# Kernel optimization log

Measured on AMD Instinct MI355X. Metric: run time of the kernel, lower is better.

The kernel has to match this reference:

```python
import jax, jax.numpy as jnp
import numpy as np

B, S, D_MODEL, H = 4, 2048, 2048, 16
HD = D_MODEL // H  # 128
ROPE_BASE = 10000.0


def apply_rope(x):
    # x: [B, H, S, HD]; interleaved-pair rotary embedding along seq axis
    s, d = x.shape[2], x.shape[3]
    inv_freq = 1.0 / (ROPE_BASE ** (jnp.arange(0, d, 2, dtype=jnp.float32) / d))  # [d/2]
    ang = jnp.arange(s, dtype=jnp.float32)[:, None] * inv_freq[None, :]  # [S, d/2]
    cos, sin = jnp.cos(ang), jnp.sin(ang)
    x0, x1 = x[..., 0::2], x[..., 1::2]  # [B,H,S,d/2]
    o0 = x0 * cos - x1 * sin
    o1 = x0 * sin + x1 * cos
    return jnp.stack([o0, o1], axis=-1).reshape(x.shape)


def setup_inputs() -> dict:
    key = jax.random.key(0)
    ks = jax.random.split(key, 5)
    sc = 1.0 / np.sqrt(D_MODEL)
    return {
        "x": jax.random.normal(ks[0], (B, S, D_MODEL), dtype=jnp.float32),
        "Wq": jax.random.normal(ks[1], (D_MODEL, D_MODEL), dtype=jnp.float32) * sc,
        "Wk": jax.random.normal(ks[2], (D_MODEL, D_MODEL), dtype=jnp.float32) * sc,
        "Wv": jax.random.normal(ks[3], (D_MODEL, D_MODEL), dtype=jnp.float32) * sc,
        "Wo": jax.random.normal(ks[4], (D_MODEL, D_MODEL), dtype=jnp.float32) * sc,
        "bo": jnp.zeros((D_MODEL,), dtype=jnp.float32),
    }


def reference(x, Wq, Wk, Wv, Wo, bo):
    b, s, _ = x.shape
    # torch Linear: y = x @ W.T (no qkv bias)
    q = (x @ Wq.T).reshape(b, s, H, HD).transpose(0, 2, 1, 3)  # [B,H,S,HD]
    k = (x @ Wk.T).reshape(b, s, H, HD).transpose(0, 2, 1, 3)
    v = (x @ Wv.T).reshape(b, s, H, HD).transpose(0, 2, 1, 3)
    q = apply_rope(q)
    k = apply_rope(k)
    scores = jnp.einsum("bhqd,bhkd->bhqk", q, k)
    causal = jnp.tril(jnp.ones((s, s), dtype=bool))
    scores = jnp.where(causal, scores, -jnp.inf)
    attn = jax.nn.softmax(scores / jnp.sqrt(jnp.float32(HD)), axis=-1)
    # dropout p=0.0 -> identity
    ctx = jnp.einsum("bhqk,bhkd->bqhd", attn, v).reshape(b, s, H * HD)
    return ctx @ Wo.T + bo
```

## Files before the change

### kernel.cpp

```cpp
#include <hip/hip_runtime.h>
#include <hip/hip_bf16.h>
#include <math.h>

#define B_  4
#define S_  2048
#define DM  2048
#define H_  16
#define HD_ 128

typedef __bf16 bf16;
typedef __bf16 bf16x4 __attribute__((ext_vector_type(4)));
typedef __bf16 bf16x8 __attribute__((ext_vector_type(8)));
typedef float  f32x4  __attribute__((ext_vector_type(4)));

__device__ __forceinline__ void gload_lds16(const bf16* g, bf16* l) {
  __builtin_amdgcn_global_load_lds(
      (const __attribute__((address_space(1))) void*)g,
      (__attribute__((address_space(3))) void*)l, 16, 0, 0);
}

__global__ void cast_f32_bf16(const float* __restrict__ src, bf16* __restrict__ dst, int n4) {
  int stride = gridDim.x * blockDim.x;
  for (int i = blockIdx.x * blockDim.x + threadIdx.x; i < n4; i += stride) {
    float4 v = reinterpret_cast<const float4*>(src)[i];
    bf16x4 o = { (bf16)v.x, (bf16)v.y, (bf16)v.z, (bf16)v.w };
    reinterpret_cast<bf16x4*>(dst)[i] = o;
  }
}

__global__ void rope_table_k(float* __restrict__ tab) {
  int idx = blockIdx.x * blockDim.x + threadIdx.x;
  if (idx >= S_ * (HD_ / 2)) return;
  int pos = idx >> 6, i = idx & 63;
  float inv = powf(10000.0f, -(2.0f * i) / (float)HD_);
  float ang = (float)pos * inv;
  tab[2 * idx]     = cosf(ang);
  tab[2 * idx + 1] = sinf(ang);
}

template<int EPI>
__global__ __launch_bounds__(512, 2)
void gemm8p(const bf16* __restrict__ A, const bf16* __restrict__ Bt,
            bf16* __restrict__ Oq, bf16* __restrict__ Ok, bf16* __restrict__ Ovt,
            float* __restrict__ Cf, const float* __restrict__ bias,
            const float* __restrict__ tab, int N, int K) {
  __shared__ char lds[131072];
  const int tid = threadIdx.x;
  const int w = tid >> 6, l = tid & 63;
  const int lr = l & 15, lg = l >> 4;
  const int wm = w >> 2, wn = w & 3;
  const int row0 = blockIdx.y * 256, col0 = blockIdx.x * 256;
  const int NT = K >> 6;

  auto stageSlot = [&](int isB, int kh, int kt2) {
    const bf16* src = isB ? (Bt + (size_t)col0 * K) : (A + (size_t)row0 * K);
    char* dstbase = (char*)lds + (kt2 & 1) * 65536 + isB * 32768 + kh * 16384;
    const int kcol = kt2 * 64 + kh * 32;
#pragma unroll
    for (int u = 0; u < 2; ++u) {
      int D = w * 2048 + u * 1024 + l * 16;
      int r = D >> 6, cb = D & 63;
      int sc = cb ^ (((r >> 1) & 3) << 4);
      gload_lds16(src + (size_t)r * K + kcol + (sc >> 1),
                  (bf16*)(dstbase + w * 2048 + u * 1024));
    }
  };

  const int swzt = ((lr >> 1) & 3) << 4;
  int offA[2][4], offB[4];
#pragma unroll
  for (int qm = 0; qm < 2; ++qm)
#pragma unroll
    for (int mi = 0; mi < 4; ++mi) {
      int r = wm * 128 + qm * 64 + mi * 16 + lr;
      offA[qm][mi] = r * 64 + ((lg * 16) ^ swzt);
    }
#pragma unroll
  for (int ni = 0; ni < 4; ++ni) {
    int r = wn * 64 + ni * 16 + lr;
    offB[ni] = 32768 + r * 64 + ((lg * 16) ^ swzt);
  }

  f32x4 acc[8][4] = {};

  stageSlot(0, 0, 0); stageSlot(1, 0, 0);
  stageSlot(0, 1, 0); stageSlot(1, 1, 0);
  if (NT > 1) { stageSlot(0, 0, 1); stageSlot(1, 0, 1); }

#pragma unroll 1
  for (int kt = 0; kt < NT; ++kt) {
    const char* bufb = (const char*)lds + (kt & 1) * 65536;
#pragma unroll
    for (int q = 0; q < 4; ++q) {
      const int qm = q & 1 ? 1 : 0;
      const int kh = q >> 1;
      const int qmm = (q == 1 || q == 3) ? 1 : 0;
      if (q == 0) {
        if (kt + 1 < NT) asm volatile("s_waitcnt vmcnt(8)" ::: "memory");
        else             asm volatile("s_waitcnt vmcnt(4)" ::: "memory");
        __builtin_amdgcn_s_barrier();
      } else if (q == 2) {
        if (kt + 1 < NT) asm volatile("s_waitcnt vmcnt(8)" ::: "memory");
        else             asm volatile("s_waitcnt vmcnt(0)" ::: "memory");
        __builtin_amdgcn_s_barrier();
      }
      const char* bb = bufb + kh * 16384;
      bf16x8 af[4], bfr[4];
#pragma unroll
      for (int mi = 0; mi < 4; ++mi)
        af[mi] = *reinterpret_cast<const bf16x8*>(bb + offA[qmm][mi]);
#pragma unroll
      for (int ni = 0; ni < 4; ++ni)
        bfr[ni] = *reinterpret_cast<const bf16x8*>(bb + offB[ni]);
      if (q < 2) { if (kt + 1 < NT) stageSlot(q & 1, 1, kt + 1); }
      else       { if (kt + 2 < NT) stageSlot(q & 1, 0, kt + 2); }
      __builtin_amdgcn_s_barrier();
      asm volatile("s_waitcnt lgkmcnt(0)" ::: "memory");
      __builtin_amdgcn_s_setprio(1);
#pragma unroll
      for (int mi = 0; mi < 4; ++mi)
#pragma unroll
        for (int ni = 0; ni < 4; ++ni)
          acc[qmm * 4 + mi][ni] =
              __builtin_amdgcn_mfma_f32_16x16x32_bf16(af[mi], bfr[ni], acc[qmm * 4 + mi][ni], 0, 0, 0);
      __builtin_amdgcn_s_setprio(0);
    }
  }

#pragma unroll
  for (int ai = 0; ai < 8; ++ai) {
    int rb = row0 + wm * 128 + ai * 16 + lg * 4;
#pragma unroll
    for (int ni = 0; ni < 4; ++ni) {
      int gc = col0 + wn * 64 + ni * 16 + lr;
      if (EPI == 1) {
#pragma unroll
        for (int j = 0; j < 4; ++j)
          Cf[(size_t)(rb + j) * N + gc] = acc[ai][ni][j] + bias[gc];
      } else {
        int reg = col0 >> 11;
        int cc = gc & 2047;
        if (reg == 2) {
          int bb2 = rb >> 11, s = rb & 2047;
          int hh = cc >> 7, dd = cc & 127;
          bf16x4 pack = { (bf16)acc[ai][ni][0], (bf16)acc[ai][ni][1],
                          (bf16)acc[ai][ni][2], (bf16)acc[ai][ni][3] };
          *reinterpret_cast<bf16x4*>(Ovt + (((size_t)(bb2 * H_ + hh) * HD_ + dd) << 11) + s) = pack;
        } else {
          bf16* Dst = (reg == 0) ? Oq : Ok;
          float scale = (reg == 0) ? 0.08838834764831845f : 1.0f;
          int i2 = (cc & 127) >> 1;
          float sgn = (lr & 1) ? 1.0f : -1.0f;
#pragma unroll
          for (int j = 0; j < 4; ++j) {
            float own = acc[ai][ni][j];
            float par = __shfl_xor(own, 1);
            int s = (rb + j) & (S_ - 1);
            float2 cs = reinterpret_cast<const float2*>(tab)[s * 64 + i2];
            Dst[(size_t)(rb + j) * 2048 + cc] = (bf16)((own * cs.x + sgn * par * cs.y) * scale);
          }
        }
      }
    }
  }
}

__global__ __launch_bounds__(512, 4)
void attn_fwd(const bf16* __restrict__ Q, const bf16* __restrict__ K,
              const bf16* __restrict__ Vt, bf16* __restrict__ O) {
  __shared__ bf16 Ks[2][64 * 128];
  __shared__ bf16 Vs[2][128 * 64];
  __shared__ bf16 Ps[8][16 * 64];
  const int tid = threadIdx.x;
  const int w = tid >> 6, l = tid & 63;
  const int lr = l & 15, lg = l >> 4;
  const int bx = blockIdx.x;
  const int h = blockIdx.y, b = blockIdx.z;
  const size_t bbase = (size_t)b * S_ * DM + (size_t)h * HD_;
  const bf16* vtb = Vt + (size_t)(b * H_ + h) * HD_ * S_;

#pragma unroll 1
  for (int pass = 0; pass < 2; ++pass) {
    const int qt = pass ? bx : (15 - bx);
    const int q0 = qt * 128 + w * 16;
    const int ktmax = 2 * qt + 1;

    bf16x8 qf[4];
#pragma unroll
    for (int kb = 0; kb < 4; ++kb)
      qf[kb] = *reinterpret_cast<const bf16x8*>(Q + bbase + (size_t)(q0 + lr) * DM + kb * 32 + lg * 8);

    float m_r = -INFINITY;
    float l_r = 0.f;
    f32x4 o[8] = {};

#pragma unroll
    for (int i = 0; i < 2; ++i) {
      int X = w * 2048 + i * 1024 + l * 16;
      int r = X >> 8, scb = (X & 255) ^ ((r & 7) << 4);
      gload_lds16(K + bbase + (size_t)r * DM + (scb >> 1), &Ks[0][(w * 2048 + i * 1024) >> 1]);
    }
#pragma unroll
    for (int i = 0; i < 2; ++i) {
      int X = w * 2048 + i * 1024 + l * 16;
      int d = X >> 7, scb = (X & 127) ^ ((d & 7) << 4);
      gload_lds16(vtb + (size_t)d * S_ + (scb >> 1), &Vs[0][(w * 2048 + i * 1024) >> 1]);
    }

    for (int kt = 0; kt <= ktmax; ++kt) {
      const int buf = kt & 1;
      if (kt < ktmax) {
        const int nk = (kt + 1) * 64;
#pragma unroll
        for (int i = 0; i < 2; ++i) {
          int X = w * 2048 + i * 1024 + l * 16;
          int r = X >> 8, scb = (X & 255) ^ ((r & 7) << 4);
          gload_lds16(K + bbase + (size_t)(nk + r) * DM + (scb >> 1),
                      &Ks[buf ^ 1][(w * 2048 + i * 1024) >> 1]);
        }
#pragma unroll
        for (int i = 0; i < 2; ++i) {
          int X = w * 2048 + i * 1024 + l * 16;
          int d = X >> 7, scb = (X & 127) ^ ((d & 7) << 4);
          gload_lds16(vtb + (size_t)d * S_ + nk + (scb >> 1),
                      &Vs[buf ^ 1][(w * 2048 + i * 1024) >> 1]);
        }
        asm volatile("s_waitcnt vmcnt(4)" ::: "memory");
      } else {
        asm volatile("s_waitcnt vmcnt(0)" ::: "memory");
      }
      __builtin_amdgcn_s_barrier();

      f32x4 sc4[4];
      __builtin_amdgcn_s_setprio(1);
#pragma unroll
      for (int cb = 0; cb < 4; ++cb) {
        sc4[cb] = f32x4{0.f, 0.f, 0.f, 0.f};
        int r = cb * 16 + lr;
#pragma unroll
        for (int kb = 0; kb < 4; ++kb) {
          int off = r * 256 + ((kb * 64 + lg * 16) ^ ((lr & 7) << 4));
          bf16x8 kf = *reinterpret_cast<const bf16x8*>((const char*)Ks[buf] + off);
          sc4[cb] = __builtin_amdgcn_mfma_f32_16x16x32_bf16(kf, qf[kb], sc4[cb], 0, 0, 0);
        }
      }
      __builtin_amdgcn_s_setprio(0);

      const int kv0 = kt * 64;
      if (kv0 + 63 > q0) {
        const int qq = q0 + lr;
#pragma unroll
        for (int cb = 0; cb < 4; ++cb)
#pragma unroll
          for (int jj = 0; jj < 4; ++jj)
            if (kv0 + cb * 16 + lg * 4 + jj > qq) sc4[cb][jj] = -INFINITY;
      }

      float tm = -INFINITY;
#pragma unroll
      for (int cb = 0; cb < 4; ++cb)
#pragma unroll
        for (int jj = 0; jj < 4; ++jj) tm = fmaxf(tm, sc4[cb][jj]);
      tm = fmaxf(tm, __shfl_xor(tm, 16));
      tm = fmaxf(tm, __shfl_xor(tm, 32));
      float mnew = fmaxf(m_r, tm);
      float sc_f = __expf(m_r - mnew);
      m_r = mnew;
      float rs = 0.f;
#pragma unroll
      for (int cb = 0; cb < 4; ++cb)
#pragma unroll
        for (int jj = 0; jj < 4; ++jj) {
          float p = __expf(sc4[cb][jj] - mnew);
          sc4[cb][jj] = p;
          rs += p;
        }
      rs += __shfl_xor(rs, 16);
      rs += __shfl_xor(rs, 32);
      l_r = l_r * sc_f + rs;

      float scO[4];
#pragma unroll
      for (int j = 0; j < 4; ++j) scO[j] = __shfl(sc_f, lg * 4 + j);
#pragma unroll
      for (int nb = 0; nb < 8; ++nb)
#pragma unroll
        for (int j = 0; j < 4; ++j) o[nb][j] *= scO[j];

#pragma unroll
      for (int cb = 0; cb < 4; ++cb) {
        bf16x4 pk = { (bf16)sc4[cb][0], (bf16)sc4[cb][1], (bf16)sc4[cb][2], (bf16)sc4[cb][3] };
        int off = lr * 128 + ((cb * 32 + lg * 8) ^ ((lr & 7) << 4));
        *reinterpret_cast<bf16x4*>((char*)Ps[w] + off) = pk;
      }

      bf16x8 pf[2];
#pragma unroll
      for (int kc = 0; kc < 2; ++kc) {
        int off = lr * 128 + ((kc * 64 + lg * 16) ^ ((lr & 7) << 4));
        pf[kc] = *reinterpret_cast<const bf16x8*>((const char*)Ps[w] + off);
      }
      __builtin_amdgcn_s_setprio(1);
#pragma unroll
      for (int nb = 0; nb < 8; ++nb) {
        int d = nb * 16 + lr;
#pragma unroll
        for (int kc = 0; kc < 2; ++kc) {
          int off = d * 128 + ((kc * 64 + lg * 16) ^ ((lr & 7) << 4));
          bf16x8 vf = *reinterpret_cast<const bf16x8*>((const char*)Vs[buf] + off);
          o[nb] = __builtin_amdgcn_mfma_f32_16x16x32_bf16(pf[kc], vf, o[nb], 0, 0, 0);
        }
      }
      __builtin_amdgcn_s_setprio(0);

      asm volatile("s_waitcnt lgkmcnt(0)" ::: "memory");
      __builtin_amdgcn_s_barrier();
    }

    float lO[4];
#pragma unroll
    for (int j = 0; j < 4; ++j) lO[j] = __shfl(l_r, lg * 4 + j);
#pragma unroll
    for (int j = 0; j < 4; ++j) {
      float inv = 1.0f / lO[j];
      size_t rowoff = bbase + (size_t)(q0 + lg * 4 + j) * DM;
#pragma unroll
      for (int nb = 0; nb < 8; ++nb)
        O[rowoff + nb * 16 + lr] = (bf16)(o[nb][j] * inv);
    }
  }
}

extern "C" void kernel_launch(void* const* d_in, const int* in_sizes, int n_in,
                              void* d_out, int out_size, void* d_ws, size_t ws_size,
                              hipStream_t stream) {
  const float* x  = (const float*)d_in[0];
  const float* Wq = (const float*)d_in[1];
  const float* Wk = (const float*)d_in[2];
  const float* Wv = (const float*)d_in[3];
  const float* Wo = (const float*)d_in[4];
  const float* bo = (const float*)d_in[5];
  float* out = (float*)d_out;

  const size_t NX = (size_t)B_ * S_ * DM;
  const size_t NW = (size_t)DM * DM;
  char* ws = (char*)d_ws;
  bf16* xb   = (bf16*)ws; ws += NX * 2;
  bf16* wqkv = (bf16*)ws; ws += 3 * NW * 2;
  bf16* wob  = (bf16*)ws; ws += NW * 2;
  bf16* qb   = (bf16*)ws; ws += NX * 2;
  bf16* kb   = (bf16*)ws; ws += NX * 2;
  bf16* vt   = (bf16*)ws; ws += NX * 2;
  bf16* ctxb = (bf16*)ws; ws += NX * 2;
  float* tab = (float*)ws; ws += (size_t)S_ * 64 * 2 * sizeof(float);

  cast_f32_bf16<<<(int)((NX / 4 + 255) / 256), 256, 0, stream>>>(x, xb, (int)(NX / 4));
  cast_f32_bf16<<<(int)((NW / 4 + 255) / 256), 256, 0, stream>>>(Wq, wqkv, (int)(NW / 4));
  cast_f32_bf16<<<(int)((NW / 4 + 255) / 256), 256, 0, stream>>>(Wk, wqkv + NW, (int)(NW / 4));
  cast_f32_bf16<<<(int)((NW / 4 + 255) / 256), 256, 0, stream>>>(Wv, wqkv + 2 * NW, (int)(NW / 4));
  cast_f32_bf16<<<(int)((NW / 4 + 255) / 256), 256, 0, stream>>>(Wo, wob, (int)(NW / 4));
  rope_table_k<<<(S_ * 64 + 255) / 256, 256, 0, stream>>>(tab);

  const int M = B_ * S_;
  gemm8p<0><<<dim3(3 * DM / 256, M / 256), 512, 0, stream>>>(
      xb, wqkv, qb, kb, vt, nullptr, nullptr, tab, 3 * DM, DM);

  attn_fwd<<<dim3(8, H_, B_), 512, 0, stream>>>(qb, kb, vt, ctxb);

  gemm8p<1><<<dim3(DM / 256, M / 256), 512, 0, stream>>>(
      ctxb, wob, nullptr, nullptr, nullptr, out, bo, nullptr, DM, DM);
}
```

Before: 438.8 us.

## Fuse casts, add XCD-aware block remapping, and lazy softmax rescaling

Merges the five f32-to-bf16 cast launches into a single grid-stride kernel. Remaps GEMM and attention block indices so neighbouring tiles land on the same XCD for better L2 reuse. Skips the online-softmax max update and output rescale when the new tile max stays within a threshold of the running max. Also drops an explicit lgkmcnt wait before the MFMA loop. The wait removal relies on the compiler inserting the needed LDS waits, and the lazy rescale allows exp values up to e^8 before renormalisation, which slightly changes numerics.

Result: faster. 418.4 us (-4.6%).

```diff
diff --git a/kernel.cpp b/kernel.cpp
--- a/kernel.cpp
+++ b/kernel.cpp
@@ -19,12 +19,28 @@
       (__attribute__((address_space(3))) void*)l, 16, 0, 0);
 }
 
-__global__ void cast_f32_bf16(const float* __restrict__ src, bf16* __restrict__ dst, int n4) {
+#define NX4 4194304
+#define NW4 1048576
+__global__ void cast_all(const float* __restrict__ x, const float* __restrict__ wq,
+                         const float* __restrict__ wk, const float* __restrict__ wv,
+                         const float* __restrict__ wo,
+                         bf16* __restrict__ xb, bf16* __restrict__ wqkv,
+                         bf16* __restrict__ wob) {
+  const int total = NX4 + 4 * NW4;
   int stride = gridDim.x * blockDim.x;
-  for (int i = blockIdx.x * blockDim.x + threadIdx.x; i < n4; i += stride) {
-    float4 v = reinterpret_cast<const float4*>(src)[i];
+  for (int i = blockIdx.x * blockDim.x + threadIdx.x; i < total; i += stride) {
+    const float* src; bf16* dst; int j;
+    if (i < NX4) { src = x; dst = xb; j = i; }
+    else {
+      int t = i - NX4; int r = t >> 20; j = t & (NW4 - 1);
+      if      (r == 0) { src = wq; dst = wqkv; }
+      else if (r == 1) { src = wk; dst = wqkv + (size_t)NW4 * 4; }
+      else if (r == 2) { src = wv; dst = wqkv + (size_t)NW4 * 8; }
+      else             { src = wo; dst = wob; }
+    }
+    float4 v = reinterpret_cast<const float4*>(src)[j];
     bf16x4 o = { (bf16)v.x, (bf16)v.y, (bf16)v.z, (bf16)v.w };
-    reinterpret_cast<bf16x4*>(dst)[i] = o;
+    reinterpret_cast<bf16x4*>(dst)[j] = o;
   }
 }
 
@@ -49,7 +65,13 @@
   const int w = tid >> 6, l = tid & 63;
   const int lr = l & 15, lg = l >> 4;
   const int wm = w >> 2, wn = w & 3;
-  const int row0 = blockIdx.y * 256, col0 = blockIdx.x * 256;
+  const int L = blockIdx.x + gridDim.x * blockIdx.y;
+  const int xcd = L & 7, s = L >> 3;
+  const int rpx = gridDim.y >> 3;
+  const int qq_ = s / gridDim.x;
+  const int by = xcd * rpx + qq_;
+  const int bx = s - qq_ * gridDim.x;
+  const int row0 = by * 256, col0 = bx * 256;
   const int NT = K >> 6;
 
   auto stageSlot = [&](int isB, int kh, int kt2) {
@@ -92,9 +114,8 @@
     const char* bufb = (const char*)lds + (kt & 1) * 65536;
 #pragma unroll
     for (int q = 0; q < 4; ++q) {
-      const int qm = q & 1 ? 1 : 0;
       const int kh = q >> 1;
-      const int qmm = (q == 1 || q == 3) ? 1 : 0;
+      const int qmm = (q & 1);
       if (q == 0) {
         if (kt + 1 < NT) asm volatile("s_waitcnt vmcnt(8)" ::: "memory");
         else             asm volatile("s_waitcnt vmcnt(4)" ::: "memory");
@@ -115,7 +136,6 @@
       if (q < 2) { if (kt + 1 < NT) stageSlot(q & 1, 1, kt + 1); }
       else       { if (kt + 2 < NT) stageSlot(q & 1, 0, kt + 2); }
       __builtin_amdgcn_s_barrier();
-      asm volatile("s_waitcnt lgkmcnt(0)" ::: "memory");
       __builtin_amdgcn_s_setprio(1);
 #pragma unroll
       for (int mi = 0; mi < 4; ++mi)
@@ -141,11 +161,11 @@
         int reg = col0 >> 11;
         int cc = gc & 2047;
         if (reg == 2) {
-          int bb2 = rb >> 11, s = rb & 2047;
+          int bb2 = rb >> 11, ss = rb & 2047;
           int hh = cc >> 7, dd = cc & 127;
           bf16x4 pack = { (bf16)acc[ai][ni][0], (bf16)acc[ai][ni][1],
                           (bf16)acc[ai][ni][2], (bf16)acc[ai][ni][3] };
-          *reinterpret_cast<bf16x4*>(Ovt + (((size_t)(bb2 * H_ + hh) * HD_ + dd) << 11) + s) = pack;
+          *reinterpret_cast<bf16x4*>(Ovt + (((size_t)(bb2 * H_ + hh) * HD_ + dd) << 11) + ss) = pack;
         } else {
           bf16* Dst = (reg == 0) ? Oq : Ok;
           float scale = (reg == 0) ? 0.08838834764831845f : 1.0f;
@@ -155,8 +175,8 @@
           for (int j = 0; j < 4; ++j) {
             float own = acc[ai][ni][j];
             float par = __shfl_xor(own, 1);
-            int s = (rb + j) & (S_ - 1);
-            float2 cs = reinterpret_cast<const float2*>(tab)[s * 64 + i2];
+            int ss = (rb + j) & (S_ - 1);
+            float2 cs = reinterpret_cast<const float2*>(tab)[ss * 64 + i2];
             Dst[(size_t)(rb + j) * 2048 + cc] = (bf16)((own * cs.x + sgn * par * cs.y) * scale);
           }
         }
@@ -174,8 +194,11 @@
   const int tid = threadIdx.x;
   const int w = tid >> 6, l = tid & 63;
   const int lr = l & 15, lg = l >> 4;
-  const int bx = blockIdx.x;
-  const int h = blockIdx.y, b = blockIdx.z;
+  const int L = blockIdx.x + 8 * (blockIdx.y + 16 * blockIdx.z);
+  const int xcd = L & 7, s = L >> 3;
+  const int p = xcd * 8 + (s & 7);
+  const int bx = s >> 3;
+  const int h = p & 15, b = p >> 4;
   const size_t bbase = (size_t)b * S_ * DM + (size_t)h * HD_;
   const bf16* vtb = Vt + (size_t)(b * H_ + h) * HD_ * S_;
 
@@ -263,29 +286,34 @@
         for (int jj = 0; jj < 4; ++jj) tm = fmaxf(tm, sc4[cb][jj]);
       tm = fmaxf(tm, __shfl_xor(tm, 16));
       tm = fmaxf(tm, __shfl_xor(tm, 32));
-      float mnew = fmaxf(m_r, tm);
-      float sc_f = __expf(m_r - mnew);
-      m_r = mnew;
+      const bool resc = !__all(tm <= m_r + 8.0f);
+      float sc_f = 1.f;
+      if (resc) {
+        float mnew = fmaxf(m_r, tm);
+        sc_f = __expf(m_r - mnew);
+        m_r = mnew;
+      }
       float rs = 0.f;
 #pragma unroll
       for (int cb = 0; cb < 4; ++cb)
 #pragma unroll
         for (int jj = 0; jj < 4; ++jj) {
-          float p = __expf(sc4[cb][jj] - mnew);
-          sc4[cb][jj] = p;
-          rs += p;
+          float pp = __expf(sc4[cb][jj] - m_r);
+          sc4[cb][jj] = pp;
+          rs += pp;
         }
       rs += __shfl_xor(rs, 16);
       rs += __shfl_xor(rs, 32);
       l_r = l_r * sc_f + rs;
-
-      float scO[4];
-#pragma unroll
-      for (int j = 0; j < 4; ++j) scO[j] = __shfl(sc_f, lg * 4 + j);
-#pragma unroll
-      for (int nb = 0; nb < 8; ++nb)
-#pragma unroll
-        for (int j = 0; j < 4; ++j) o[nb][j] *= scO[j];
+      if (resc) {
+        float scO[4];
+#pragma unroll
+        for (int j = 0; j < 4; ++j) scO[j] = __shfl(sc_f, lg * 4 + j);
+#pragma unroll
+        for (int nb = 0; nb < 8; ++nb)
+#pragma unroll
+          for (int j = 0; j < 4; ++j) o[nb][j] *= scO[j];
+      }
 
 #pragma unroll
       for (int cb = 0; cb < 4; ++cb) {
@@ -354,11 +382,7 @@
   bf16* ctxb = (bf16*)ws; ws += NX * 2;
   float* tab = (float*)ws; ws += (size_t)S_ * 64 * 2 * sizeof(float);
 
-  cast_f32_bf16<<<(int)((NX / 4 + 255) / 256), 256, 0, stream>>>(x, xb, (int)(NX / 4));
-  cast_f32_bf16<<<(int)((NW / 4 + 255) / 256), 256, 0, stream>>>(Wq, wqkv, (int)(NW / 4));
-  cast_f32_bf16<<<(int)((NW / 4 + 255) / 256), 256, 0, stream>>>(Wk, wqkv + NW, (int)(NW / 4));
-  cast_f32_bf16<<<(int)((NW / 4 + 255) / 256), 256, 0, stream>>>(Wv, wqkv + 2 * NW, (int)(NW / 4));
-  cast_f32_bf16<<<(int)((NW / 4 + 255) / 256), 256, 0, stream>>>(Wo, wob, (int)(NW / 4));
+  cast_all<<<2048, 256, 0, stream>>>(x, Wq, Wk, Wv, Wo, xb, wqkv, wob);
   rope_table_k<<<(S_ * 64 + 255) / 256, 256, 0, stream>>>(tab);
 
   const int M = B_ * S_;
```
